# Kernel optimization log

Measured on AMD Instinct MI355X. Metric: run time of the kernel, lower is better.

Reference implementation:

```python
import jax, jax.numpy as jnp
import numpy as np

B, K, N, D = 2, 384, 4096, 1024      # batch, filtered spans, all spans, dim_span
H, L, DD, NB = 150, 12, 20, 10       # scorer hidden, n_labels, dist emb dim, n buckets
REL_PROP, RESIDUAL, CTXT_FF = 2, True, True


def setup_inputs() -> dict:
    key = jax.random.key(0)
    ks = jax.random.split(key, 14)
    span_vecs = jax.random.normal(ks[0], (B, K, D), dtype=jnp.float32)
    all_span_vecs = jax.random.normal(ks[1], (B, N, D), dtype=jnp.float32)
    span_begin = jnp.sort(jax.random.randint(ks[2], (B, K), 0, 512), axis=-1)
    span_end = span_begin + jax.random.randint(ks[3], (B, K), 0, 8)
    span_lengths = jnp.full((B,), (K * 9) // 10, dtype=jnp.int32)
    valid = jnp.arange(K)[None, :] < span_lengths[:, None]
    square_mask = (valid[:, :, None] & valid[:, None, :]).astype(jnp.float32)
    prune_indices = jnp.sort(jax.random.randint(ks[4], (B, K), 0, N), axis=-1)
    sequence_lengths = jnp.full((B,), 512, dtype=jnp.int32)
    p = lambda k, sh: jax.random.normal(k, sh, dtype=jnp.float32) * 0.02
    return {
        'span_vecs': span_vecs, 'all_span_vecs': all_span_vecs,
        'span_begin': span_begin, 'span_end': span_end,
        'square_mask': square_mask, 'prune_indices': prune_indices,
        'span_lengths': span_lengths, 'sequence_lengths': sequence_lengths,
        'Wl': p(ks[5], (D, H)), 'bl': jnp.zeros((H,), jnp.float32),
        'Wr': p(ks[6], (D, H)), 'br': jnp.zeros((H,), jnp.float32),
        'dist_emb': p(ks[7], (NB, DD)),
        'Wd': p(ks[8], (DD, H)), 'bd': jnp.zeros((H,), jnp.float32),
        'Wo': p(ks[9], (H, L)), 'bo': jnp.zeros((L,), jnp.float32),
        'Wff1': p(ks[10], (3 * D, D)), 'Wff2': p(ks[11], (D, D)),
        'Wg': p(ks[12], (2 * D, D)), 'bg': jnp.zeros((D,), jnp.float32),
    }


def _bucket(d):
    # coref-style distance buckets: 0..4 exact, then log2 buckets up to NB-1
    da = jnp.abs(d)
    lg = jnp.floor(jnp.log2(jnp.maximum(da, 1).astype(jnp.float32))).astype(jnp.int32) + 3
    return jnp.where(da <= 4, da, jnp.minimum(lg, NB - 1)).astype(jnp.int32)


def _scorer(u, span_begin, span_end, Wl, bl, Wr, br, dist_emb, Wd, bd, Wo, bo):
    # OptFFpairs: pairwise FF scorer, [B,K,D] -> [B,K,K,L] (dropout = identity, eval mode)
    l = u @ Wl + bl                                          # [B,K,H]
    r = u @ Wr + br                                          # [B,K,H]
    dist = span_begin[:, None, :] - span_end[:, :, None]     # [B,K,K]
    d = dist_emb[_bucket(dist)] @ Wd + bd                    # [B,K,K,H]
    h = jax.nn.relu(l[:, :, None, :] + r[:, None, :, :] + d)
    return h @ Wo + bo                                       # [B,K,K,L]


def _forward(span_vecs, square_mask, span_begin, span_end,
             Wl, bl, Wr, br, dist_emb, Wd, bd, Wo, bo, Wff1, Wff2, Wg, bg):
    u = span_vecs
    scores = _scorer(u, span_begin, span_end, Wl, bl, Wr, br, dist_emb, Wd, bd, Wo, bo)
    for _ in range(REL_PROP):
        probs1 = jax.nn.sigmoid(scores.max(-1)) * square_mask       # [B,K,K]
        probs2 = jnp.swapaxes(probs1, 1, 2)
        ctxt1 = jnp.einsum('bij,bjd->bid', probs1, u) / (probs1.sum(-1) + 1e-7)[..., None]
        ctxt2 = jnp.einsum('bij,bjd->bid', probs2, u) / (probs2.sum(-1) + 1e-7)[..., None]
        if CTXT_FF:
            ctxt = jnp.tanh(jnp.concatenate((u, ctxt1, ctxt2), -1) @ Wff1) @ Wff2
        else:
            ctxt = ctxt1 + ctxt2
        g = jax.nn.sigmoid(jnp.concatenate((u, ctxt), -1) @ Wg + bg)  # MyGate
        u = g * u + (1.0 - g) * ctxt
        new_scores = _scorer(u, span_begin, span_end, Wl, bl, Wr, br, dist_emb, Wd, bd, Wo, bo)
        scores = scores + new_scores if RESIDUAL else new_scores
    return u, scores


def reference(span_vecs, all_span_vecs, span_begin, span_end, square_mask,
              prune_indices, span_lengths, sequence_lengths,
              Wl, bl, Wr, br, dist_emb, Wd, bd, Wo, bo, Wff1, Wff2, Wg, bg):
    u, scores = _forward(span_vecs, square_mask, span_begin, span_end,
                         Wl, bl, Wr, br, dist_emb, Wd, bd, Wo, bo, Wff1, Wff2, Wg, bg)
    # overwrite_spans: write updated filtered span vecs back into all-span tensor
    valid = jnp.arange(K)[None, :] < span_lengths[:, None]          # [B,K]
    bidx = jnp.broadcast_to(jnp.arange(B)[:, None], (B, K))
    cur = all_span_vecs[bidx, prune_indices]                        # [B,K,D]
    vals = jnp.where(valid[..., None], u, cur)                      # invalid -> no-op write
    update_all = all_span_vecs.at[bidx, prune_indices].set(vals)
    return update_all, u, scores
```

## Files before the change

### kernel.cpp

```cpp
#include <hip/hip_runtime.h>
#include <cmath>

#define B_ 2
#define K_ 384
#define N_ 4096
#define D_ 1024
#define H_ 150
#define L_ 12
#define NB_ 10
#define LDW_S 164

typedef unsigned short u16;
typedef __bf16 bf16x8 __attribute__((ext_vector_type(8)));
typedef float f32x4 __attribute__((ext_vector_type(4)));

__device__ __forceinline__ u16 f2bf(float f){
  unsigned u = __builtin_bit_cast(unsigned, f);
  unsigned r = (u + 0x7FFFu + ((u >> 16) & 1u)) >> 16;
  return (u16)r;
}
__device__ __forceinline__ float bf2f(u16 h){
  unsigned u = ((unsigned)h) << 16;
  return __builtin_bit_cast(float, u);
}
__device__ __forceinline__ int bucketf(int d){
  int da = d < 0 ? -d : d;
  if (da <= 4) return da;
  int lg = 31 - __clz(da);
  int v = lg + 3;
  return v > NB_ - 1 ? NB_ - 1 : v;
}

__global__ void transpose_f2bf(const float* __restrict__ in, u16* __restrict__ out,
                               int Kd, int Nd, int ostride){
  __shared__ float t[32][33];
  int bx = blockIdx.x * 32, by = blockIdx.y * 32;
  int tx = threadIdx.x, ty = threadIdx.y;
  for (int i = 0; i < 32; i += 8){
    int k = by + ty + i, n = bx + tx;
    t[ty + i][tx] = (k < Kd && n < Nd) ? in[(size_t)k * Nd + n] : 0.f;
  }
  __syncthreads();
  for (int i = 0; i < 32; i += 8){
    int n = bx + ty + i, k = by + tx;
    if (n < Nd && k < Kd) out[(size_t)n * ostride + k] = f2bf(t[tx][ty + i]);
  }
}

__global__ void transpose_bf(const u16* __restrict__ in, u16* __restrict__ out){
  __shared__ u16 t[32][34];
  int b = blockIdx.z;
  const u16* I = in + (size_t)b * K_ * D_;
  u16* O = out + (size_t)b * D_ * K_;
  int bx = blockIdx.x * 32, by = blockIdx.y * 32;
  int tx = threadIdx.x, ty = threadIdx.y;
  for (int i = 0; i < 32; i += 8) t[ty + i][tx] = I[(size_t)(by + ty + i) * D_ + bx + tx];
  __syncthreads();
  for (int i = 0; i < 32; i += 8) O[(size_t)(bx + ty + i) * K_ + by + tx] = t[tx][ty + i];
}

__global__ void small_setup(const float* __restrict__ dist_emb, const float* __restrict__ Wd,
                            const float* __restrict__ bd, const float* __restrict__ bl,
                            const float* __restrict__ br, const float* __restrict__ Wo,
                            float* __restrict__ dWg, float* __restrict__ blr,
                            u16* __restrict__ woT){
  int tid = threadIdx.x;
  for (int idx = tid; idx < NB_ * H_; idx += 256){
    int nb = idx / H_, h = idx - nb * H_;
    float s = bd[h];
    for (int dd = 0; dd < 20; ++dd) s += dist_emb[nb * 20 + dd] * Wd[dd * H_ + h];
    dWg[idx] = s;
  }
  for (int idx = tid; idx < H_; idx += 256){
    blr[idx] = bl[idx];
    blr[H_ + idx] = br[idx];
  }
  for (int idx = tid; idx < 16 * 160; idx += 256){
    int l = idx / 160, t = idx - l * 160;
    float w = (l < L_ && t < H_) ? Wo[t * L_ + l] : 0.f;
    woT[idx] = f2bf(w);
  }
}

__global__ void cvt_f32_bf16(const float* __restrict__ in, u16* __restrict__ out, int n){
  int idx = (blockIdx.x * 256 + threadIdx.x) * 4;
  if (idx < n){
    float4 v = *(const float4*)(in + idx);
    ushort4 o;
    o.x = f2bf(v.x); o.y = f2bf(v.y); o.z = f2bf(v.z); o.w = f2bf(v.w);
    *(ushort4*)(out + idx) = o;
  }
}

__global__ void init_lr(const float* __restrict__ blr, float* __restrict__ lr){
  int idx = blockIdx.x * 256 + threadIdx.x;
  if (idx >= (B_ * K_) * 320) return;
  int col = idx % 320;
  float v = 0.f;
  if (col < 150) v = blr[col];
  else if (col >= 160 && col < 310) v = blr[150 + (col - 160)];
  lr[idx] = v;
}

__global__ __launch_bounds__(256)
void gemm_part_atomic32(const u16* __restrict__ A0, const u16* __restrict__ A1,
                        const u16* __restrict__ A2, const u16* __restrict__ BT,
                        int Ktot, int klen, float* __restrict__ Out, int ldo){
  __shared__ u16 As[32][72];
  __shared__ u16 Bs[64][72];
  int tid = threadIdx.x;
  int m0 = blockIdx.x * 32, n0 = blockIdx.y * 64;
  int s = blockIdx.z;
  int kbeg = s * klen, kend = kbeg + klen;
  int wave = tid >> 6, lane = tid & 63;
  int wm = wave >> 1, wn = wave & 1;
  int q = lane >> 4, mr = lane & 15;
  f32x4 acc[2] = {{0.f,0.f,0.f,0.f},{0.f,0.f,0.f,0.f}};
  const u16* Achunks[3] = {A0, A1, A2};
  for (int k0 = kbeg; k0 < kend; k0 += 64){
    const u16* Ap = Achunks[k0 >> 10] + (k0 & 1023);
    {
      int row = tid >> 3, c8 = tid & 7;
      *(uint4*)&As[row][c8 * 8] = *(const uint4*)&Ap[(size_t)(m0 + row) * 1024 + c8 * 8];
    }
    for (int c = tid; c < 512; c += 256){
      int row = c >> 3, c8 = c & 7;
      *(uint4*)&Bs[row][c8 * 8] = *(const uint4*)&BT[(size_t)(n0 + row) * Ktot + k0 + c8 * 8];
    }
    __syncthreads();
#pragma unroll
    for (int ks = 0; ks < 64; ks += 32){
      bf16x8 a  = *(const bf16x8*)&As[wm * 16 + mr][ks + q * 8];
      bf16x8 b0 = *(const bf16x8*)&Bs[wn * 32 + mr][ks + q * 8];
      bf16x8 b1 = *(const bf16x8*)&Bs[wn * 32 + 16 + mr][ks + q * 8];
      acc[0] = __builtin_amdgcn_mfma_f32_16x16x32_bf16(a, b0, acc[0], 0, 0, 0);
      acc[1] = __builtin_amdgcn_mfma_f32_16x16x32_bf16(a, b1, acc[1], 0, 0, 0);
    }
    __syncthreads();
  }
#pragma unroll
  for (int nt = 0; nt < 2; ++nt){
    int col = n0 + wn * 32 + nt * 16 + mr;
#pragma unroll
    for (int r = 0; r < 4; ++r){
      int row = m0 + wm * 16 + q * 4 + r;
      atomicAdd(&Out[(size_t)row * ldo + col], acc[nt][r]);
    }
  }
}

__global__ __launch_bounds__(256)
void gemm_epi(float* __restrict__ accF, int n,
              const float* __restrict__ bias, int mode,
              float* __restrict__ outF, u16* __restrict__ outH,
              const float* __restrict__ uin, const u16* __restrict__ ctxtin){
  int idx = blockIdx.x * 256 + threadIdx.x;
  if (idx >= n) return;
  float ssum = accF[idx];
  accF[idx] = 0.f;
  if (mode == 1){
    outH[idx] = f2bf(tanhf(ssum));
  } else if (mode == 2){
    outH[idx] = f2bf(ssum);
  } else {
    int col = idx & 1023;
    float g = 1.f / (1.f + expf(-(ssum + bias[col])));
    float uo = uin[idx];
    float ct = bf2f(ctxtin[idx]);
    float un = ct + g * (uo - ct);
    outF[idx] = un;
    outH[idx] = f2bf(un);
  }
}

__global__ __launch_bounds__(256)
void ctxt_mfma(const u16* __restrict__ Pbf, const u16* __restrict__ PTbf,
               const u16* __restrict__ uT, const float* __restrict__ rowsum,
               const float* __restrict__ colsum, u16* __restrict__ c1,
               u16* __restrict__ c2){
  __shared__ u16 As[32][72];
  __shared__ u16 Bs[64][72];
  int z = blockIdx.z, b = z >> 1, which = z & 1;
  const u16* A = (which ? PTbf : Pbf) + (size_t)b * K_ * K_;
  const u16* BT = uT + (size_t)b * D_ * K_;
  const float* sums = (which ? colsum : rowsum) + b * K_;
  u16* out = which ? c2 : c1;
  int tid = threadIdx.x;
  int m0 = blockIdx.x * 32, n0 = blockIdx.y * 64;
  int wave = tid >> 6, lane = tid & 63;
  int wm = wave >> 1, wn = wave & 1;
  int q = lane >> 4, mr = lane & 15;
  f32x4 acc[2] = {{0.f,0.f,0.f,0.f},{0.f,0.f,0.f,0.f}};
  for (int k0 = 0; k0 < K_; k0 += 64){
    {
      int row = tid >> 3, c8 = tid & 7;
      *(uint4*)&As[row][c8 * 8] = *(const uint4*)&A[(size_t)(m0 + row) * K_ + k0 + c8 * 8];
    }
    for (int c = tid; c < 512; c += 256){
      int row = c >> 3, c8 = c & 7;
      *(uint4*)&Bs[row][c8 * 8] = *(const uint4*)&BT[(size_t)(n0 + row) * K_ + k0 + c8 * 8];
    }
    __syncthreads();
#pragma unroll
    for (int ks = 0; ks < 64; ks += 32){
      bf16x8 a  = *(const bf16x8*)&As[wm * 16 + mr][ks + q * 8];
      bf16x8 b0 = *(const bf16x8*)&Bs[wn * 32 + mr][ks + q * 8];
      bf16x8 b1 = *(const bf16x8*)&Bs[wn * 32 + 16 + mr][ks + q * 8];
      acc[0] = __builtin_amdgcn_mfma_f32_16x16x32_bf16(a, b0, acc[0], 0, 0, 0);
      acc[1] = __builtin_amdgcn_mfma_f32_16x16x32_bf16(a, b1, acc[1], 0, 0, 0);
    }
    __syncthreads();
  }
#pragma unroll
  for (int nt = 0; nt < 2; ++nt){
    int col = n0 + wn * 32 + nt * 16 + mr;
#pragma unroll
    for (int r = 0; r < 4; ++r){
      int row = m0 + wm * 16 + q * 4 + r;
      float w = 1.f / (sums[row] + 1e-7f);
      out[((size_t)(b * K_ + row)) * D_ + col] = f2bf(acc[nt][r] * w);
    }
  }
}

__global__ __launch_bounds__(256)
void scorer_kernel(const float* __restrict__ lr, const float* __restrict__ dWg,
                   const u16* __restrict__ woT, const float* __restrict__ bo,
                   const int* __restrict__ span_begin, const int* __restrict__ span_end,
                   float* __restrict__ scores, float* __restrict__ maxS, int accumulate){
  __shared__ float ldw[NB_ * LDW_S];
  __shared__ u16 h_s[4][16][168];
  int i = blockIdx.x, jblk = blockIdx.y, b = blockIdx.z;
  int tid = threadIdx.x;
  int row_i = b * K_ + i;
  int se = span_end[row_i];
  for (int e = tid; e < NB_ * LDW_S; e += 256){
    int nb = e / LDW_S, t = e - nb * LDW_S;
    ldw[e] = (t < H_) ? (lr[(size_t)row_i * 320 + t] + dWg[nb * H_ + t]) : 0.f;
  }
  int wave = tid >> 6, lane = tid & 63;
  int q = lane >> 4, mr = lane & 15;
  bf16x8 wo_frag[5];
#pragma unroll
  for (int kk = 0; kk < 5; ++kk)
    wo_frag[kk] = *(const bf16x8*)&woT[mr * 160 + kk * 32 + q * 8];
  for (int e = lane; e < 16 * 5; e += 64){
    int row = e / 5, w5 = e - row * 5;
    *(unsigned*)&h_s[wave][row][150 + w5 * 2] = 0u;
  }
  float bov = (mr < L_) ? bo[mr] : 0.f;
  int rt = lane >> 2, tq = lane & 3;
  __syncthreads();
#pragma unroll
  for (int p = 0; p < 2; ++p){
    int j0w = jblk * 128 + wave * 32 + p * 16;
    {
      int j = j0w + rt;
      int bk = bucketf(span_begin[b * K_ + j] - se);
      const float2* rr = (const float2*)(lr + (size_t)(b * K_ + j) * 320 + 160);
      const float2* lw = (const float2*)(ldw + bk * LDW_S);
      u16* hrow = &h_s[wave][rt][0];
      int pp0 = tq * 19;
      float2 rbuf[19];
#pragma unroll
      for (int s = 0; s < 19; ++s) rbuf[s] = rr[pp0 + s];
#pragma unroll
      for (int s = 0; s < 19; ++s){
        int pp = pp0 + s;
        float2 lv = lw[pp];
        __bf16 h0 = (__bf16)fmaxf(lv.x + rbuf[s].x, 0.f);
        __bf16 h1 = (__bf16)fmaxf(lv.y + rbuf[s].y, 0.f);
        unsigned pk = (unsigned)__builtin_bit_cast(u16, h0) |
                      ((unsigned)__builtin_bit_cast(u16, h1) << 16);
        *(unsigned*)&hrow[pp * 2] = pk;
      }
    }
    f32x4 acc = {0.f, 0.f, 0.f, 0.f};
#pragma unroll
    for (int kk = 0; kk < 5; ++kk){
      bf16x8 a = *(const bf16x8*)&h_s[wave][mr][kk * 32 + q * 8];
      acc = __builtin_amdgcn_mfma_f32_16x16x32_bf16(a, wo_frag[kk], acc, 0, 0, 0);
    }
#pragma unroll
    for (int r = 0; r < 4; ++r){
      int j = j0w + q * 4 + r;
      float v = -3.0e38f;
      if (mr < L_){
        size_t addr = ((size_t)row_i * K_ + j) * L_ + mr;
        v = acc[r] + bov;
        if (accumulate) v += scores[addr];
        scores[addr] = v;
      }
      float mx = v;
      mx = fmaxf(mx, __shfl_xor(mx, 1, 16));
      mx = fmaxf(mx, __shfl_xor(mx, 2, 16));
      mx = fmaxf(mx, __shfl_xor(mx, 4, 16));
      mx = fmaxf(mx, __shfl_xor(mx, 8, 16));
      if (mr == 0) maxS[(size_t)row_i * K_ + j] = mx;
    }
  }
}

__global__ __launch_bounds__(384)
void probs_kernel(const float* __restrict__ maxS, const float* __restrict__ mask,
                  u16* __restrict__ pbf, u16* __restrict__ pTbf,
                  float* __restrict__ rowsum, float* __restrict__ colsum){
  int i = blockIdx.x, b = blockIdx.y, j = threadIdx.x;
  size_t base = (size_t)(b * K_ + i) * K_ + j;
  float m = maxS[base];
  float p = mask[base] / (1.f + expf(-m));
  u16 ph = f2bf(p);
  pbf[base] = ph;
  pTbf[((size_t)b * K_ + j) * K_ + i] = ph;
  atomicAdd(&colsum[b * K_ + j], p);
  __shared__ float red[6];
  float s = p;
  for (int o = 32; o > 0; o >>= 1) s += __shfl_down(s, o, 64);
  if ((j & 63) == 0) red[j >> 6] = s;
  __syncthreads();
  if (j == 0){
    float tot = 0.f;
    for (int w = 0; w < 6; ++w) tot += red[w];
    rowsum[b * K_ + i] = tot;
  }
}

__global__ void copy_f4(const float4* __restrict__ src, float4* __restrict__ dst, int n){
  int g = blockIdx.x * 256 + threadIdx.x;
  if (g < n) dst[g] = src[g];
}

__global__ void scatter_kernel(const float* __restrict__ u, const int* __restrict__ prune,
                               const int* __restrict__ span_len, float* __restrict__ outA){
  int blk = blockIdx.x;
  int b = blk / K_, k = blk - b * K_;
  int idx = prune[b * K_ + k];
  bool valid = k < span_len[b];
  bool winner = (k == K_ - 1) || (prune[b * K_ + k + 1] != idx);
  if (!(valid && winner)) return;
  const float4* src = (const float4*)(u + ((size_t)b * K_ + k) * D_);
  float4* dst = (float4*)(outA + ((size_t)b * N_ + idx) * D_);
  for (int t = threadIdx.x; t < D_ / 4; t += blockDim.x) dst[t] = src[t];
}

extern "C" void kernel_launch(void* const* d_in, const int* in_sizes, int n_in,
                              void* d_out, int out_size, void* d_ws, size_t ws_size,
                              hipStream_t stream){
  const float* span_vecs = (const float*)d_in[0];
  const float* all_span  = (const float*)d_in[1];
  const int*   span_begin = (const int*)d_in[2];
  const int*   span_end   = (const int*)d_in[3];
  const float* mask       = (const float*)d_in[4];
  const int*   prune      = (const int*)d_in[5];
  const int*   span_len   = (const int*)d_in[6];
  const float* Wl  = (const float*)d_in[8];
  const float* bl  = (const float*)d_in[9];
  const float* Wr  = (const float*)d_in[10];
  const float* br  = (const float*)d_in[11];
  const float* dist_emb = (const float*)d_in[12];
  const float* Wd  = (const float*)d_in[13];
  const float* bd  = (const float*)d_in[14];
  const float* Wo  = (const float*)d_in[15];
  const float* bo  = (const float*)d_in[16];
  const float* Wff1 = (const float*)d_in[17];
  const float* Wff2 = (const float*)d_in[18];
  const float* Wg  = (const float*)d_in[19];
  const float* bg  = (const float*)d_in[20];

  float* outA = (float*)d_out;
  float* outU = outA + (size_t)B_ * N_ * D_;
  float* outS = outU + (size_t)B_ * K_ * D_;

  char* base = (char*)d_ws;
  size_t off = 0;
  auto alloc = [&](size_t bytes) -> void* {
    void* p = base + off;
    off = (off + bytes + 255) & ~((size_t)255);
    return p;
  };
  u16* WlrT  = (u16*)alloc((size_t)320 * 1024 * sizeof(u16));
  u16* Wff1T = (u16*)alloc((size_t)1024 * 3072 * sizeof(u16));
  u16* Wff2T = (u16*)alloc((size_t)1024 * 1024 * sizeof(u16));
  u16* WgT   = (u16*)alloc((size_t)1024 * 2048 * sizeof(u16));
  float* dWg = (float*)alloc(NB_ * H_ * sizeof(float));
  float* blr = (float*)alloc(300 * sizeof(float));
  u16* woT   = (u16*)alloc((size_t)16 * 160 * sizeof(u16));
  float* lr  = (float*)alloc((size_t)B_ * K_ * 320 * sizeof(float));
  float* maxS  = (float*)alloc((size_t)B_ * K_ * K_ * sizeof(float));
  u16* pbf   = (u16*)alloc((size_t)B_ * K_ * K_ * sizeof(u16));
  u16* pTbf  = (u16*)alloc((size_t)B_ * K_ * K_ * sizeof(u16));
  u16* uTbf  = (u16*)alloc((size_t)B_ * D_ * K_ * sizeof(u16));
  float* rowsum = (float*)alloc(B_ * K_ * sizeof(float));
  float* colsum = (float*)alloc(B_ * K_ * sizeof(float));
  u16* ubf0 = (u16*)alloc((size_t)B_ * K_ * D_ * sizeof(u16));
  u16* ubf1 = (u16*)alloc((size_t)B_ * K_ * D_ * sizeof(u16));
  u16* c1bf = (u16*)alloc((size_t)B_ * K_ * D_ * sizeof(u16));
  u16* c2bf = (u16*)alloc((size_t)B_ * K_ * D_ * sizeof(u16));
  u16* tbf  = (u16*)alloc((size_t)B_ * K_ * D_ * sizeof(u16));
  u16* ctxtbf = (u16*)alloc((size_t)B_ * K_ * D_ * sizeof(u16));
  float* uA = (float*)alloc((size_t)B_ * K_ * D_ * sizeof(float));
  float* accF = (float*)alloc((size_t)B_ * K_ * D_ * sizeof(float));
  u16* ubf[2] = {ubf0, ubf1};
  (void)ws_size; (void)in_sizes; (void)n_in; (void)out_size;

  dim3 tb(32, 8);
  (void)hipMemsetAsync(WlrT, 0, (size_t)320 * 1024 * sizeof(u16), stream);
  transpose_f2bf<<<dim3(5, 32), tb, 0, stream>>>(Wl, WlrT, 1024, 150, 1024);
  transpose_f2bf<<<dim3(5, 32), tb, 0, stream>>>(Wr, WlrT + (size_t)160 * 1024, 1024, 150, 1024);
  transpose_f2bf<<<dim3(32, 96), tb, 0, stream>>>(Wff1, Wff1T, 3072, 1024, 3072);
  transpose_f2bf<<<dim3(32, 32), tb, 0, stream>>>(Wff2, Wff2T, 1024, 1024, 1024);
  transpose_f2bf<<<dim3(32, 64), tb, 0, stream>>>(Wg, WgT, 2048, 1024, 2048);
  small_setup<<<1, 256, 0, stream>>>(dist_emb, Wd, bd, bl, br, Wo, dWg, blr, woT);
  cvt_f32_bf16<<<768, 256, 0, stream>>>(span_vecs, ubf[0], B_ * K_ * D_);
  (void)hipMemsetAsync(accF, 0, (size_t)B_ * K_ * D_ * sizeof(float), stream);

  init_lr<<<960, 256, 0, stream>>>(blr, lr);
  gemm_part_atomic32<<<dim3(24, 5, 8), 256, 0, stream>>>(ubf[0], nullptr, nullptr, WlrT,
                                                         1024, 128, lr, 320);
  scorer_kernel<<<dim3(K_, 3, B_), 256, 0, stream>>>(lr, dWg, woT, bo, span_begin, span_end,
                                                     outS, maxS, 0);

  const float* ucurF = span_vecs;
  int cb = 0;
  float* unexts[2] = {uA, outU};
  for (int it = 0; it < 2; ++it){
    (void)hipMemsetAsync(colsum, 0, B_ * K_ * sizeof(float), stream);
    probs_kernel<<<dim3(K_, B_), 384, 0, stream>>>(maxS, mask, pbf, pTbf, rowsum, colsum);
    transpose_bf<<<dim3(32, 12, B_), tb, 0, stream>>>(ubf[cb], uTbf);
    ctxt_mfma<<<dim3(12, 16, 2 * B_), 256, 0, stream>>>(pbf, pTbf, uTbf, rowsum, colsum,
                                                        c1bf, c2bf);
    gemm_part_atomic32<<<dim3(24, 16, 4), 256, 0, stream>>>(ubf[cb], c1bf, c2bf, Wff1T,
                                                            3072, 768, accF, 1024);
    gemm_epi<<<3072, 256, 0, stream>>>(accF, B_ * K_ * D_, nullptr, 1,
                                       nullptr, tbf, nullptr, nullptr);
    gemm_part_atomic32<<<dim3(24, 16, 4), 256, 0, stream>>>(tbf, nullptr, nullptr, Wff2T,
                                                            1024, 256, accF, 1024);
    gemm_epi<<<3072, 256, 0, stream>>>(accF, B_ * K_ * D_, nullptr, 2,
                                       nullptr, ctxtbf, nullptr, nullptr);
    gemm_part_atomic32<<<dim3(24, 16, 4), 256, 0, stream>>>(ubf[cb], ctxtbf, nullptr, WgT,
                                                            2048, 512, accF, 1024);
    float* unext = unexts[it];
    gemm_epi<<<3072, 256, 0, stream>>>(accF, B_ * K_ * D_, bg, 3,
                                       unext, ubf[1 - cb], ucurF, ctxtbf);
    cb = 1 - cb;
    ucurF = unext;
    init_lr<<<960, 256, 0, stream>>>(blr, lr);
    gemm_part_atomic32<<<dim3(24, 5, 8), 256, 0, stream>>>(ubf[cb], nullptr, nullptr, WlrT,
                                                           1024, 128, lr, 320);
    scorer_kernel<<<dim3(K_, 3, B_), 256, 0, stream>>>(lr, dWg, woT, bo, span_begin, span_end,
                                                       outS, maxS, 1);
  }

  copy_f4<<<8192, 256, 0, stream>>>((const float4*)all_span, (float4*)outA, (B_ * N_ * D_) / 4);
  scatter_kernel<<<B_ * K_, 256, 0, stream>>>(ucurF, prune, span_len, outA);
}
```

Measured before the change: 504.4 us.

## Fuse GEMM epilogues via last-block counters and fold probs into scorer

Split-K GEMMs now count finished K-slices per output tile with an atomic counter, and the last block applies the tanh, identity or gate epilogue itself. This removes the separate elementwise epilogue launches and their full reread of the accumulator. The sigmoid-probability, transpose and row/column-sum computation moves into the scorer kernel, which drops the maxS buffer and the probs kernel. The cost is extra thread fences, counter atomics, more rowsum atomics and scattered transposed stores from the scorer. Skipping the probs work on the final scorer call is valid because nothing reads those probabilities afterwards.

```diff
diff --git a/kernel.cpp b/kernel.cpp
--- a/kernel.cpp
+++ b/kernel.cpp
@@ -150,27 +150,83 @@
 }
 
 __global__ __launch_bounds__(256)
-void gemm_epi(float* __restrict__ accF, int n,
-              const float* __restrict__ bias, int mode,
-              float* __restrict__ outF, u16* __restrict__ outH,
-              const float* __restrict__ uin, const u16* __restrict__ ctxtin){
-  int idx = blockIdx.x * 256 + threadIdx.x;
-  if (idx >= n) return;
-  float ssum = accF[idx];
-  accF[idx] = 0.f;
-  if (mode == 1){
-    outH[idx] = f2bf(tanhf(ssum));
-  } else if (mode == 2){
-    outH[idx] = f2bf(ssum);
-  } else {
-    int col = idx & 1023;
-    float g = 1.f / (1.f + expf(-(ssum + bias[col])));
-    float uo = uin[idx];
-    float ct = bf2f(ctxtin[idx]);
-    float un = ct + g * (uo - ct);
-    outF[idx] = un;
-    outH[idx] = f2bf(un);
-  }
+void gemm_fused(const u16* __restrict__ A0, const u16* __restrict__ A1,
+                const u16* __restrict__ A2, const u16* __restrict__ BT,
+                int Ktot, int klen, float* __restrict__ accF,
+                int* __restrict__ ctr, int S, int mode,
+                const float* __restrict__ bias, float* __restrict__ outF,
+                u16* __restrict__ outH, const float* __restrict__ uin,
+                const u16* __restrict__ ctxtin){
+  __shared__ u16 As[32][72];
+  __shared__ u16 Bs[64][72];
+  int tid = threadIdx.x;
+  int m0 = blockIdx.x * 32, n0 = blockIdx.y * 64;
+  int s = blockIdx.z;
+  int kbeg = s * klen, kend = kbeg + klen;
+  int wave = tid >> 6, lane = tid & 63;
+  int wm = wave >> 1, wn = wave & 1;
+  int q = lane >> 4, mr = lane & 15;
+  f32x4 acc[2] = {{0.f,0.f,0.f,0.f},{0.f,0.f,0.f,0.f}};
+  const u16* Achunks[3] = {A0, A1, A2};
+  for (int k0 = kbeg; k0 < kend; k0 += 64){
+    const u16* Ap = Achunks[k0 >> 10] + (k0 & 1023);
+    {
+      int row = tid >> 3, c8 = tid & 7;
+      *(uint4*)&As[row][c8 * 8] = *(const uint4*)&Ap[(size_t)(m0 + row) * 1024 + c8 * 8];
+    }
+    for (int c = tid; c < 512; c += 256){
+      int row = c >> 3, c8 = c & 7;
+      *(uint4*)&Bs[row][c8 * 8] = *(const uint4*)&BT[(size_t)(n0 + row) * Ktot + k0 + c8 * 8];
+    }
+    __syncthreads();
+#pragma unroll
+    for (int ks = 0; ks < 64; ks += 32){
+      bf16x8 a  = *(const bf16x8*)&As[wm * 16 + mr][ks + q * 8];
+      bf16x8 b0 = *(const bf16x8*)&Bs[wn * 32 + mr][ks + q * 8];
+      bf16x8 b1 = *(const bf16x8*)&Bs[wn * 32 + 16 + mr][ks + q * 8];
+      acc[0] = __builtin_amdgcn_mfma_f32_16x16x32_bf16(a, b0, acc[0], 0, 0, 0);
+      acc[1] = __builtin_amdgcn_mfma_f32_16x16x32_bf16(a, b1, acc[1], 0, 0, 0);
+    }
+    __syncthreads();
+  }
+#pragma unroll
+  for (int nt = 0; nt < 2; ++nt){
+    int col = n0 + wn * 32 + nt * 16 + mr;
+#pragma unroll
+    for (int r = 0; r < 4; ++r){
+      int row = m0 + wm * 16 + q * 4 + r;
+      atomicAdd(&accF[(size_t)row * 1024 + col], acc[nt][r]);
+    }
+  }
+  __threadfence();
+  __shared__ int is_last;
+  int cidx = blockIdx.x * gridDim.y + blockIdx.y;
+  if (tid == 0){
+    int old = atomicAdd(&ctr[cidx], 1);
+    is_last = (old == S - 1);
+  }
+  __syncthreads();
+  if (!is_last) return;
+  __threadfence();
+  for (int e = tid; e < 32 * 64; e += 256){
+    int rr = e >> 6, cc = e & 63;
+    size_t idx = (size_t)(m0 + rr) * 1024 + (n0 + cc);
+    float ssum = accF[idx];
+    accF[idx] = 0.f;
+    if (mode == 1){
+      outH[idx] = f2bf(tanhf(ssum));
+    } else if (mode == 2){
+      outH[idx] = f2bf(ssum);
+    } else {
+      float g = 1.f / (1.f + expf(-(ssum + bias[(int)(idx & 1023)])));
+      float uo = uin[idx];
+      float ct = bf2f(ctxtin[idx]);
+      float un = ct + g * (uo - ct);
+      outF[idx] = un;
+      outH[idx] = f2bf(un);
+    }
+  }
+  if (tid == 0) ctr[cidx] = 0;
 }
 
 __global__ __launch_bounds__(256)
@@ -227,7 +283,10 @@
 void scorer_kernel(const float* __restrict__ lr, const float* __restrict__ dWg,
                    const u16* __restrict__ woT, const float* __restrict__ bo,
                    const int* __restrict__ span_begin, const int* __restrict__ span_end,
-                   float* __restrict__ scores, float* __restrict__ maxS, int accumulate){
+                   float* __restrict__ scores, int accumulate,
+                   const float* __restrict__ mask, u16* __restrict__ pbf,
+                   u16* __restrict__ pTbf, float* __restrict__ rowsum,
+                   float* __restrict__ colsum, int wprobs){
   __shared__ float ldw[NB_ * LDW_S];
   __shared__ u16 h_s[4][16][168];
   int i = blockIdx.x, jblk = blockIdx.y, b = blockIdx.z;
@@ -250,6 +309,7 @@
   }
   float bov = (mr < L_) ? bo[mr] : 0.f;
   int rt = lane >> 2, tq = lane & 3;
+  float rsum = 0.f;
   __syncthreads();
 #pragma unroll
   for (int p = 0; p < 2; ++p){
@@ -296,33 +356,18 @@
       mx = fmaxf(mx, __shfl_xor(mx, 2, 16));
       mx = fmaxf(mx, __shfl_xor(mx, 4, 16));
       mx = fmaxf(mx, __shfl_xor(mx, 8, 16));
-      if (mr == 0) maxS[(size_t)row_i * K_ + j] = mx;
-    }
-  }
-}
-
-__global__ __launch_bounds__(384)
-void probs_kernel(const float* __restrict__ maxS, const float* __restrict__ mask,
-                  u16* __restrict__ pbf, u16* __restrict__ pTbf,
-                  float* __restrict__ rowsum, float* __restrict__ colsum){
-  int i = blockIdx.x, b = blockIdx.y, j = threadIdx.x;
-  size_t base = (size_t)(b * K_ + i) * K_ + j;
-  float m = maxS[base];
-  float p = mask[base] / (1.f + expf(-m));
-  u16 ph = f2bf(p);
-  pbf[base] = ph;
-  pTbf[((size_t)b * K_ + j) * K_ + i] = ph;
-  atomicAdd(&colsum[b * K_ + j], p);
-  __shared__ float red[6];
-  float s = p;
-  for (int o = 32; o > 0; o >>= 1) s += __shfl_down(s, o, 64);
-  if ((j & 63) == 0) red[j >> 6] = s;
-  __syncthreads();
-  if (j == 0){
-    float tot = 0.f;
-    for (int w = 0; w < 6; ++w) tot += red[w];
-    rowsum[b * K_ + i] = tot;
-  }
+      if (wprobs && mr == 0){
+        size_t pb = (size_t)row_i * K_ + j;
+        float pp = mask[pb] / (1.f + expf(-mx));
+        u16 ph = f2bf(pp);
+        pbf[pb] = ph;
+        pTbf[((size_t)b * K_ + j) * K_ + i] = ph;
+        atomicAdd(&colsum[b * K_ + j], pp);
+        rsum += pp;
+      }
+    }
+  }
+  if (wprobs && mr == 0) atomicAdd(&rowsum[row_i], rsum);
 }
 
 __global__ void copy_f4(const float4* __restrict__ src, float4* __restrict__ dst, int n){
@@ -385,13 +430,13 @@
   float* dWg = (float*)alloc(NB_ * H_ * sizeof(float));
   float* blr = (float*)alloc(300 * sizeof(float));
   u16* woT   = (u16*)alloc((size_t)16 * 160 * sizeof(u16));
+  int* gctr  = (int*)alloc(384 * sizeof(int));
   float* lr  = (float*)alloc((size_t)B_ * K_ * 320 * sizeof(float));
-  float* maxS  = (float*)alloc((size_t)B_ * K_ * K_ * sizeof(float));
   u16* pbf   = (u16*)alloc((size_t)B_ * K_ * K_ * sizeof(u16));
   u16* pTbf  = (u16*)alloc((size_t)B_ * K_ * K_ * sizeof(u16));
   u16* uTbf  = (u16*)alloc((size_t)B_ * D_ * K_ * sizeof(u16));
-  float* rowsum = (float*)alloc(B_ * K_ * sizeof(float));
-  float* colsum = (float*)alloc(B_ * K_ * sizeof(float));
+  float* rowsum = (float*)alloc((size_t)2 * B_ * K_ * sizeof(float));
+  float* colsum = rowsum + B_ * K_;
   u16* ubf0 = (u16*)alloc((size_t)B_ * K_ * D_ * sizeof(u16));
   u16* ubf1 = (u16*)alloc((size_t)B_ * K_ * D_ * sizeof(u16));
   u16* c1bf = (u16*)alloc((size_t)B_ * K_ * D_ * sizeof(u16));
@@ -413,42 +458,45 @@
   small_setup<<<1, 256, 0, stream>>>(dist_emb, Wd, bd, bl, br, Wo, dWg, blr, woT);
   cvt_f32_bf16<<<768, 256, 0, stream>>>(span_vecs, ubf[0], B_ * K_ * D_);
   (void)hipMemsetAsync(accF, 0, (size_t)B_ * K_ * D_ * sizeof(float), stream);
+  (void)hipMemsetAsync(gctr, 0, 384 * sizeof(int), stream);
 
   init_lr<<<960, 256, 0, stream>>>(blr, lr);
   gemm_part_atomic32<<<dim3(24, 5, 8), 256, 0, stream>>>(ubf[0], nullptr, nullptr, WlrT,
                                                          1024, 128, lr, 320);
+  (void)hipMemsetAsync(rowsum, 0, (size_t)2 * B_ * K_ * sizeof(float), stream);
   scorer_kernel<<<dim3(K_, 3, B_), 256, 0, stream>>>(lr, dWg, woT, bo, span_begin, span_end,
-                                                     outS, maxS, 0);
+                                                     outS, 0, mask, pbf, pTbf, rowsum, colsum, 1);
 
   const float* ucurF = span_vecs;
   int cb = 0;
   float* unexts[2] = {uA, outU};
   for (int it = 0; it < 2; ++it){
-    (void)hipMemsetAsync(colsum, 0, B_ * K_ * sizeof(float), stream);
-    probs_kernel<<<dim3(K_, B_), 384, 0, stream>>>(maxS, mask, pbf, pTbf, rowsum, colsum);
     transpose_bf<<<dim3(32, 12, B_), tb, 0, stream>>>(ubf[cb], uTbf);
     ctxt_mfma<<<dim3(12, 16, 2 * B_), 256, 0, stream>>>(pbf, pTbf, uTbf, rowsum, colsum,
                                                         c1bf, c2bf);
-    gemm_part_atomic32<<<dim3(24, 16, 4), 256, 0, stream>>>(ubf[cb], c1bf, c2bf, Wff1T,
-                                                            3072, 768, accF, 1024);
-    gemm_epi<<<3072, 256, 0, stream>>>(accF, B_ * K_ * D_, nullptr, 1,
-                                       nullptr, tbf, nullptr, nullptr);
-    gemm_part_atomic32<<<dim3(24, 16, 4), 256, 0, stream>>>(tbf, nullptr, nullptr, Wff2T,
-                                                            1024, 256, accF, 1024);
-    gemm_epi<<<3072, 256, 0, stream>>>(accF, B_ * K_ * D_, nullptr, 2,
-                                       nullptr, ctxtbf, nullptr, nullptr);
-    gemm_part_atomic32<<<dim3(24, 16, 4), 256, 0, stream>>>(ubf[cb], ctxtbf, nullptr, WgT,
-                                                            2048, 512, accF, 1024);
+    gemm_fused<<<dim3(24, 16, 4), 256, 0, stream>>>(ubf[cb], c1bf, c2bf, Wff1T,
+                                                    3072, 768, accF, gctr, 4, 1,
+                                                    nullptr, nullptr, tbf, nullptr, nullptr);
+    gemm_fused<<<dim3(24, 16, 4), 256, 0, stream>>>(tbf, nullptr, nullptr, Wff2T,
+                                                    1024, 256, accF, gctr, 4, 2,
+                                                    nullptr, nullptr, ctxtbf, nullptr, nullptr);
     float* unext = unexts[it];
-    gemm_epi<<<3072, 256, 0, stream>>>(accF, B_ * K_ * D_, bg, 3,
-                                       unext, ubf[1 - cb], ucurF, ctxtbf);
+    gemm_fused<<<dim3(24, 16, 4), 256, 0, stream>>>(ubf[cb], ctxtbf, nullptr, WgT,
+                                                    2048, 512, accF, gctr, 4, 3,
+                                                    bg, unext, ubf[1 - cb], ucurF, ctxtbf);
     cb = 1 - cb;
     ucurF = unext;
     init_lr<<<960, 256, 0, stream>>>(blr, lr);
     gemm_part_atomic32<<<dim3(24, 5, 8), 256, 0, stream>>>(ubf[cb], nullptr, nullptr, WlrT,
                                                            1024, 128, lr, 320);
-    scorer_kernel<<<dim3(K_, 3, B_), 256, 0, stream>>>(lr, dWg, woT, bo, span_begin, span_end,
-                                                       outS, maxS, 1);
+    if (it == 0){
+      (void)hipMemsetAsync(rowsum, 0, (size_t)2 * B_ * K_ * sizeof(float), stream);
+      scorer_kernel<<<dim3(K_, 3, B_), 256, 0, stream>>>(lr, dWg, woT, bo, span_begin, span_end,
+                                                         outS, 1, mask, pbf, pTbf, rowsum, colsum, 1);
+    } else {
+      scorer_kernel<<<dim3(K_, 3, B_), 256, 0, stream>>>(lr, dWg, woT, bo, span_begin, span_end,
+                                                         outS, 1, mask, pbf, pTbf, rowsum, colsum, 0);
+    }
   }
 
   copy_f4<<<8192, 256, 0, stream>>>((const float4*)all_span, (float4*)outA, (B_ * N_ * D_) / 4);
```

Result: slower. 1.332 ms (+164.0%).
